# Kernel optimization log

Measured on AMD Instinct MI355X. Metric: run time of the kernel, lower is better.

Reference implementation:

```python
import jax, jax.numpy as jnp
import numpy as np

B, S, D, H, L, E, FF = 16, 1024, 384, 8, 3, 8, 768
DH = D // H
TOP_K = 2


def _ln(x, s, b):
    m = x.mean(-1, keepdims=True)
    v = x.var(-1, keepdims=True)
    return (x - m) * jax.lax.rsqrt(v + 1e-5) * s + b


def setup_inputs() -> dict:
    key = jax.random.key(0)
    ks = jax.random.split(key, 12)
    def n(k, shp, scale=0.02):
        return jax.random.normal(k, shp, jnp.float32) * scale
    return dict(
        x=jax.random.normal(ks[0], (B, S, 1), jnp.float32),
        proj_w=n(ks[1], (1, D)), proj_b=jnp.zeros((D,), jnp.float32),
        qkv_w=n(ks[2], (L, D, 3 * D)), qkv_b=jnp.zeros((L, 3 * D), jnp.float32),
        out_w=n(ks[3], (L, D, D)), out_b=jnp.zeros((L, D), jnp.float32),
        n1_s=jnp.ones((L, D), jnp.float32), n1_b=jnp.zeros((L, D), jnp.float32),
        n2_s=jnp.ones((L, D), jnp.float32), n2_b=jnp.zeros((L, D), jnp.float32),
        gate_w=n(ks[4], (L, D, E)),
        e_w1=n(ks[5], (L, E, D, FF)), e_b1=jnp.zeros((L, E, FF), jnp.float32),
        e_w2=n(ks[6], (L, E, FF, D)), e_b2=jnp.zeros((L, E, D), jnp.float32),
        att_w=n(ks[7], (D,)), att_b=jnp.zeros((), jnp.float32),
        head_w=n(ks[8], (D, 1)), head_b=jnp.zeros((1,), jnp.float32),
    )


def reference(x, proj_w, proj_b, qkv_w, qkv_b, out_w, out_b,
              n1_s, n1_b, n2_s, n2_b, gate_w, e_w1, e_b1, e_w2, e_b2,
              att_w, att_b, head_w, head_b):
    # feature projection: [B,S,1] -> [B,S,D]
    h = x @ proj_w + proj_b
    total_moe = jnp.zeros((), h.dtype)
    scale = np.float32(1.0 / np.sqrt(DH))
    for l in range(L):
        # --- pre-norm multi-head self-attention ---
        xn = _ln(h, n1_s[l], n1_b[l])
        qkv = xn @ qkv_w[l] + qkv_b[l]
        q, k, v = jnp.split(qkv, 3, axis=-1)
        q = q.reshape(B, S, H, DH)
        k = k.reshape(B, S, H, DH)
        v = v.reshape(B, S, H, DH)
        attn = jax.nn.softmax(jnp.einsum('bqhd,bkhd->bhqk', q, k) * scale, axis=-1)
        ao = jnp.einsum('bhqk,bkhd->bqhd', attn, v).reshape(B, S, D)
        h = h + (ao @ out_w[l] + out_b[l])
        # --- pre-norm top-2 gated MoE FFN ---
        xn2 = _ln(h, n2_s[l], n2_b[l])
        probs = jax.nn.softmax(xn2 @ gate_w[l], axis=-1)            # [B,S,E]
        topv, topi = jax.lax.top_k(probs, TOP_K)
        gates = topv / topv.sum(-1, keepdims=True)                  # renormalized top-2
        full = (jax.nn.one_hot(topi, E, dtype=h.dtype) * gates[..., None]).sum(-2)  # [B,S,E]
        moe_out = jnp.zeros_like(h)
        for e in range(E):  # fixed small expert loop
            ye = jax.nn.relu(xn2 @ e_w1[l, e] + e_b1[l, e]) @ e_w2[l, e] + e_b2[l, e]
            moe_out = moe_out + full[..., e:e + 1] * ye
        h = h + moe_out
        # switch-style load-balancing aux loss
        importance = probs.reshape(-1, E).mean(0)
        load = (full > 0).astype(h.dtype).reshape(-1, E).mean(0)
        total_moe = total_moe + E * jnp.sum(importance * load)
    w = jax.nn.softmax(h @ att_w + att_b, axis=1)                   # [B,S]
    pooled = jnp.einsum('bs,bsd->bd', w, h)
    rul = pooled @ head_w + head_b                                  # [B,1]
    return rul, total_moe
```

## Files before the change

### kernel.cpp

```cpp
#include <hip/hip_runtime.h>
#include <hip/hip_bf16.h>
#include <math.h>

#define TOKENS 16384
#define DMODEL 384
#define SEQ 1024
#define NHEAD 8
#define DHEAD 48
#define NEXP 8
#define FFDIM 768
#define NL 3

typedef __bf16 bf16x8 __attribute__((ext_vector_type(8)));
typedef __bf16 bf16x4 __attribute__((ext_vector_type(4)));
typedef float f32x4 __attribute__((ext_vector_type(4)));

__global__ void finalize_kernel(const int* __restrict__ counts_all,
                                const float* __restrict__ sp_all, float* __restrict__ out) {
  float tm = 0.f;
  for (int l = 0; l < NL; l++) {
    float t = 0.f;
    for (int e = 0; e < NEXP; e++)
      t += sp_all[l * NEXP + e] * (float)counts_all[l * NEXP + e];
    tm += (float)NEXP * t / ((float)TOKENS * (float)TOKENS);
  }
  out[16] = tm;
}

__global__ __launch_bounds__(256) void proj_kernel(const float* __restrict__ x,
    const float* __restrict__ pw, const float* __restrict__ pb, float* __restrict__ h) {
  int i = blockIdx.x * 256 + threadIdx.x;
  int t = i / DMODEL;
  int d = i - t * DMODEL;
  h[i] = x[t] * pw[d] + pb[d];
}

__global__ __launch_bounds__(256) void convw_kernel(const float* __restrict__ src,
    __bf16* __restrict__ dst, int K, int N) {
  __shared__ float t[32][33];
  size_t boff = (size_t)blockIdx.z * K * N;
  src += boff; dst += boff;
  int k0 = blockIdx.y * 32, n0 = blockIdx.x * 32;
  int tx = threadIdx.x & 31, ty = threadIdx.x >> 5;
#pragma unroll
  for (int i = 0; i < 32; i += 8) t[ty + i][tx] = src[(size_t)(k0 + ty + i) * N + n0 + tx];
  __syncthreads();
#pragma unroll
  for (int i = 0; i < 32; i += 8)
    dst[(size_t)(n0 + ty + i) * K + k0 + tx] = (__bf16)t[tx][ty + i];
}

__global__ __launch_bounds__(384) void ln_kernel(const float* __restrict__ src,
    __bf16* __restrict__ dst, const float* __restrict__ gs, const float* __restrict__ gb,
    int* __restrict__ zc, float* __restrict__ zs) {
  int row = blockIdx.x, tid = threadIdx.x;
  if (zc && row == 0 && tid < NEXP) { zc[tid] = 0; zs[tid] = 0.f; }
  float v = src[(size_t)row * DMODEL + tid];
  float sum = v, sq = v * v;
#pragma unroll
  for (int off = 32; off; off >>= 1) { sum += __shfl_xor(sum, off); sq += __shfl_xor(sq, off); }
  __shared__ float rs[6], rq[6];
  __shared__ float smean, sinv;
  int wid = tid >> 6;
  if ((tid & 63) == 0) { rs[wid] = sum; rq[wid] = sq; }
  __syncthreads();
  if (tid == 0) {
    float S = 0.f, Q = 0.f;
    for (int w = 0; w < 6; w++) { S += rs[w]; Q += rq[w]; }
    float mean = S / (float)DMODEL;
    float var = Q / (float)DMODEL - mean * mean;
    smean = mean; sinv = rsqrtf(var + 1e-5f);
  }
  __syncthreads();
  dst[(size_t)row * DMODEL + tid] = (__bf16)((v - smean) * sinv * gs[tid] + gb[tid]);
}

__global__ __launch_bounds__(384) void lncomb_kernel(float* __restrict__ h,
    const __bf16* __restrict__ ab, __bf16* __restrict__ dst,
    const float* __restrict__ gs, const float* __restrict__ gb) {
  int row = blockIdx.x, tid = threadIdx.x;
  size_t idx = (size_t)row * DMODEL + tid;
  float v = h[idx] + (float)ab[idx] + (float)ab[(size_t)TOKENS * DMODEL + idx];
  h[idx] = v;
  float sum = v, sq = v * v;
#pragma unroll
  for (int off = 32; off; off >>= 1) { sum += __shfl_xor(sum, off); sq += __shfl_xor(sq, off); }
  __shared__ float rs[6], rq[6];
  __shared__ float smean, sinv;
  int wid = tid >> 6;
  if ((tid & 63) == 0) { rs[wid] = sum; rq[wid] = sq; }
  __syncthreads();
  if (tid == 0) {
    float S = 0.f, Q = 0.f;
    for (int w = 0; w < 6; w++) { S += rs[w]; Q += rq[w]; }
    float mean = S / (float)DMODEL;
    float var = Q / (float)DMODEL - mean * mean;
    smean = mean; sinv = rsqrtf(var + 1e-5f);
  }
  __syncthreads();
  dst[idx] = (__bf16)((v - smean) * sinv * gs[tid] + gb[tid]);
}

template<int MODE>
__global__ __launch_bounds__(256) void mgemm_kernel(
    const __bf16* __restrict__ Abf, const __bf16* __restrict__ Wt,
    const float* __restrict__ bias, float* __restrict__ Cf, __bf16* __restrict__ Cb,
    __bf16* __restrict__ pQ, __bf16* __restrict__ pK, __bf16* __restrict__ pV,
    const int* __restrict__ counts,
    const int* __restrict__ tok_list, const float* __restrict__ gate_list,
    int N, int K) {
  int e = 0, cnt = 0, base = 0;
  const int* tl = nullptr;
  int m0 = blockIdx.y * 128;
  int n0 = blockIdx.x * 128;
  if constexpr (MODE == 2 || MODE == 3) {
    e = blockIdx.z;
    cnt = counts[e];
    if (m0 >= cnt) return;
    for (int i = 0; i < NEXP; i++) {
      int ci = counts[i];
      if (i < e) base += (ci + 63) & ~63;
    }
    tl = tok_list + e * TOKENS;
    Wt += (size_t)e * N * K;
    bias += (size_t)e * N;
  }
  __shared__ __align__(16) __bf16 smem[128][130];
  auto Bs = reinterpret_cast<__bf16(*)[72]>(&smem[0][0]);
  int tid = threadIdx.x;
  int w = tid >> 6, lane = tid & 63, c = lane & 15, g = lane >> 4;
  int arow[4], acol[4];
#pragma unroll
  for (int i = 0; i < 4; i++) {
    int chunk = tid + 256 * i;
    arow[i] = chunk >> 3;
    acol[i] = (chunk & 7) * 8;
  }
  int r1 = w * 32 + c, r2 = r1 + 16;
  long tokf0, tokf1;
  {
    int mr1 = m0 + r1, mr2 = m0 + r2;
    if constexpr (MODE == 2) {
      tokf0 = (mr1 < cnt) ? (long)(tl[mr1] & 0xFFFF) : -1;
      tokf1 = (mr2 < cnt) ? (long)(tl[mr2] & 0xFFFF) : -1;
    } else if constexpr (MODE == 3) {
      tokf0 = (mr1 < cnt) ? (long)(base + mr1) : -1;
      tokf1 = (mr2 < cnt) ? (long)(base + mr2) : -1;
    } else {
      tokf0 = mr1; tokf1 = mr2;
    }
  }
  f32x4 acc[2][8];
#pragma unroll
  for (int m = 0; m < 2; m++)
#pragma unroll
    for (int n = 0; n < 8; n++) { acc[m][n][0] = 0.f; acc[m][n][1] = 0.f; acc[m][n][2] = 0.f; acc[m][n][3] = 0.f; }

  bf16x8 rb[4];
  bf16x8 af0a = {}, af0b = {}, af1a = {}, af1b = {};
  int nk = K >> 6;
#pragma unroll
  for (int i = 0; i < 4; i++)
    rb[i] = *(const bf16x8*)&Wt[(size_t)(n0 + arow[i]) * K + acol[i]];
  if (tokf0 >= 0) {
    af0a = *(const bf16x8*)&Abf[(size_t)tokf0 * K + g * 8];
    af0b = *(const bf16x8*)&Abf[(size_t)tokf0 * K + 32 + g * 8];
  }
  if (tokf1 >= 0) {
    af1a = *(const bf16x8*)&Abf[(size_t)tokf1 * K + g * 8];
    af1b = *(const bf16x8*)&Abf[(size_t)tokf1 * K + 32 + g * 8];
  }
  for (int kt = 0; kt < nk; kt++) {
#pragma unroll
    for (int i = 0; i < 4; i++)
      *(bf16x8*)&Bs[arow[i]][acol[i]] = rb[i];
    __syncthreads();
    int k0 = (kt + 1) << 6;
    if (kt + 1 < nk) {
#pragma unroll
      for (int i = 0; i < 4; i++)
        rb[i] = *(const bf16x8*)&Wt[(size_t)(n0 + arow[i]) * K + k0 + acol[i]];
    }
#pragma unroll
    for (int n = 0; n < 8; n++) {
      bf16x8 b0 = *(const bf16x8*)&Bs[n * 16 + c][g * 8];
      acc[0][n] = __builtin_amdgcn_mfma_f32_16x16x32_bf16(af0a, b0, acc[0][n], 0, 0, 0);
      acc[1][n] = __builtin_amdgcn_mfma_f32_16x16x32_bf16(af1a, b0, acc[1][n], 0, 0, 0);
    }
#pragma unroll
    for (int n = 0; n < 8; n++) {
      bf16x8 b1 = *(const bf16x8*)&Bs[n * 16 + c][32 + g * 8];
      acc[0][n] = __builtin_amdgcn_mfma_f32_16x16x32_bf16(af0b, b1, acc[0][n], 0, 0, 0);
      acc[1][n] = __builtin_amdgcn_mfma_f32_16x16x32_bf16(af1b, b1, acc[1][n], 0, 0, 0);
    }
    if (kt + 1 < nk) {
      if (tokf0 >= 0) {
        af0a = *(const bf16x8*)&Abf[(size_t)tokf0 * K + k0 + g * 8];
        af0b = *(const bf16x8*)&Abf[(size_t)tokf0 * K + k0 + 32 + g * 8];
      }
      if (tokf1 >= 0) {
        af1a = *(const bf16x8*)&Abf[(size_t)tokf1 * K + k0 + g * 8];
        af1b = *(const bf16x8*)&Abf[(size_t)tokf1 * K + k0 + 32 + g * 8];
      }
    }
    __syncthreads();
  }
  if constexpr (MODE == 1) {
#pragma unroll
    for (int m = 0; m < 2; m++) {
      int row = w * 32 + m * 16 + 4 * g;
#pragma unroll
      for (int n = 0; n < 8; n++) {
        int col = n0 + n * 16 + c;
        float bv = bias[col];
#pragma unroll
        for (int r = 0; r < 4; r++)
          Cf[(size_t)(m0 + row + r) * N + col] += acc[m][n][r] + bv;
      }
    }
  } else if constexpr (MODE == 0) {
    __bf16* Ct = &smem[0][0];
    const int CSTR = 130;
    int which = n0 / 384;
    int rem0 = n0 - which * 384;
#pragma unroll
    for (int m = 0; m < 2; m++) {
      int row = w * 32 + m * 16 + 4 * g;
#pragma unroll
      for (int n = 0; n < 8; n++) {
        int col = n * 16 + c;
        float bv = bias[n0 + col];
#pragma unroll
        for (int r = 0; r < 4; r++) {
          float v = acc[m][n][r] + bv;
          if (which == 0) v *= 0.20823510262f;
          Ct[(row + r) * CSTR + col] = (__bf16)v;
        }
      }
    }
    __syncthreads();
    int b0 = m0 >> 10, sbase = m0 & 1023;
    if (which < 2) {
      __bf16* dstbuf = (which == 0) ? pQ : pK;
#pragma unroll
      for (int it = 0; it < 4; it++) {
        int ch = it * 256 + tid;
        int row = ch >> 3, seg = ch & 7;
        int rem = rem0 + seg * 16;
        int hd = rem / 48, d = rem - hd * 48;
        size_t bh = (size_t)(b0 * 8 + hd);
        __bf16* dst = &dstbuf[(bh * 1024 + sbase + row) * 48 + d];
        const __bf16* srcl = &Ct[row * CSTR + seg * 16];
        *(bf16x8*)&dst[0] = *(const bf16x8*)&srcl[0];
        *(bf16x8*)&dst[8] = *(const bf16x8*)&srcl[8];
      }
    } else {
      int col = tid >> 1, half = tid & 1;
      int rem = rem0 + col;
      int hd = rem / 48, d = rem - hd * 48;
      size_t bh = (size_t)(b0 * 8 + hd);
      __bf16* dst = &pV[(bh * 48 + d) * 1024 + sbase + half * 64];
      const __bf16* srcc = &Ct[(half * 64) * CSTR + col];
#pragma unroll
      for (int i8 = 0; i8 < 8; i8++) {
        bf16x8 vv;
#pragma unroll
        for (int j = 0; j < 8; j++) vv[j] = srcc[(i8 * 8 + j) * CSTR];
        *(bf16x8*)&dst[i8 * 8] = vv;
      }
    }
  } else {
    __bf16* Ct = &smem[0][0];
    const int CSTR = 130;
    float rowg[2][4];
    if constexpr (MODE == 3) {
#pragma unroll
      for (int m = 0; m < 2; m++)
#pragma unroll
        for (int r = 0; r < 4; r++) {
          int row = m0 + w * 32 + m * 16 + 4 * g + r;
          rowg[m][r] = (row < cnt) ? gate_list[e * TOKENS + row] : 0.f;
        }
    }
#pragma unroll
    for (int m = 0; m < 2; m++) {
      int row = w * 32 + m * 16 + 4 * g;
#pragma unroll
      for (int n = 0; n < 8; n++) {
        int col = n * 16 + c;
        float bv = bias[n0 + col];
#pragma unroll
        for (int r = 0; r < 4; r++) {
          float v = acc[m][n][r] + bv;
          if constexpr (MODE == 2) v = fmaxf(v, 0.f);
          else v *= rowg[m][r];
          Ct[(row + r) * CSTR + col] = (__bf16)v;
        }
      }
    }
    __syncthreads();
    int row = tid >> 1, half = tid & 1;
    int mr = m0 + row;
    if (mr < cnt) {
      const __bf16* srcl = &Ct[row * CSTR + half * 64];
      __bf16* dst;
      if constexpr (MODE == 2) {
        dst = &Cb[(size_t)(base + mr) * N + n0 + half * 64];
      } else {
        int entry = tl[mr];
        int t = entry & 0xFFFF, a = entry >> 16;
        dst = &Cb[((size_t)a * TOKENS + t) * DMODEL + n0 + half * 64];
      }
#pragma unroll
      for (int i = 0; i < 8; i++) *(bf16x8*)&dst[i * 8] = *(const bf16x8*)&srcl[i * 8];
    }
  }
}

__global__ __launch_bounds__(256) void combine_kernel(float* __restrict__ h,
    const __bf16* __restrict__ ab) {
  size_t i = ((size_t)blockIdx.x * 256 + threadIdx.x) * 8;
  bf16x8 a0 = *(const bf16x8*)&ab[i];
  bf16x8 a1 = *(const bf16x8*)&ab[(size_t)TOKENS * DMODEL + i];
  float* hp = h + i;
#pragma unroll
  for (int j = 0; j < 8; j++) hp[j] += (float)a0[j] + (float)a1[j];
}

__global__ __launch_bounds__(256, 4) void attn_kernel(const __bf16* __restrict__ Qh,
    const __bf16* __restrict__ Kh, const __bf16* __restrict__ VTh,
    __bf16* __restrict__ ao) {
  __shared__ __align__(16) __bf16 Ks[64][72];
  __shared__ __align__(16) __bf16 Vt[48][72];
  __shared__ __align__(16) __bf16 Ps[4][2][16][72];
  int bh = blockIdx.x;
  int q0 = blockIdx.y * 128;
  int tid = threadIdx.x;
  int w = tid >> 6, lane = tid & 63, c = lane & 15, g = lane >> 4;

  for (int i = tid; i < 192; i += 256) {
    int row = i / 3, seg = i - row * 3;
    bf16x8 z = {};
    *(bf16x8*)&Ks[row][48 + seg * 8] = z;
  }

  const __bf16* qrowA = Qh + ((size_t)bh * 1024 + q0 + w * 16 + c) * 48;
  const __bf16* qrowB = qrowA + 64 * 48;
  bf16x8 qb0a = *(const bf16x8*)&qrowA[g * 8];
  bf16x8 qb0b = *(const bf16x8*)&qrowB[g * 8];
  bf16x8 qb1a = {}, qb1b = {};
  if (g < 2) {
    qb1a = *(const bf16x8*)&qrowA[32 + g * 8];
    qb1b = *(const bf16x8*)&qrowB[32 + g * 8];
  }

  const __bf16* kb = Kh + (size_t)bh * 1024 * 48;
  const __bf16* vb = VTh + (size_t)bh * 48 * 1024;

  int r0 = tid / 6, p0 = tid - r0 * 6;
  __bf16* dst0 = &Ks[r0][p0 * 8];
  int off0 = r0 * 48 + p0 * 8;
  int e1 = tid + 256;
  __bf16* dst1; int off1; bool v1;
  if (e1 < 384) { int r = e1 / 6, p = e1 - r * 6; dst1 = &Ks[r][p * 8]; off1 = r * 48 + p * 8; v1 = false; }
  else          { int i = e1 - 384; int d = i >> 3, p = i & 7; dst1 = &Vt[d][p * 8]; off1 = d * 1024 + p * 8; v1 = true; }
  int i2 = tid + 512 - 384;
  int d2 = i2 >> 3, p2 = i2 & 7;
  __bf16* dst2 = &Vt[d2][p2 * 8];
  int off2 = d2 * 1024 + p2 * 8;

  f32x4 accA[3] = {}, accB[3] = {};
  f32x4 laccA = {}, laccB = {};
  bf16x8 ones;
#pragma unroll
  for (int j = 0; j < 8; j++) ones[j] = (__bf16)1.0f;

  for (int kt = 0; kt < 16; kt++) {
    __syncthreads();
    const __bf16* kbt = kb + (size_t)kt * 3072;
    const __bf16* vbt = vb + kt * 64;
    *(bf16x8*)dst0 = *(const bf16x8*)(kbt + off0);
    *(bf16x8*)dst1 = *(const bf16x8*)((v1 ? vbt : kbt) + off1);
    *(bf16x8*)dst2 = *(const bf16x8*)(vbt + off2);
    __syncthreads();

#pragma unroll
    for (int f = 0; f < 4; f++) {
      bf16x8 ka0 = *(const bf16x8*)&Ks[f * 16 + c][g * 8];
      bf16x8 ka1 = *(const bf16x8*)&Ks[f * 16 + c][32 + g * 8];
      f32x4 za = {}, zb = {};
      za = __builtin_amdgcn_mfma_f32_16x16x32_bf16(ka0, qb0a, za, 0, 0, 0);
      f32x4 sa = __builtin_amdgcn_mfma_f32_16x16x32_bf16(ka1, qb1a, za, 0, 0, 0);
      zb = __builtin_amdgcn_mfma_f32_16x16x32_bf16(ka0, qb0b, zb, 0, 0, 0);
      f32x4 sb = __builtin_amdgcn_mfma_f32_16x16x32_bf16(ka1, qb1b, zb, 0, 0, 0);
      bf16x4 pka = { (__bf16)__builtin_amdgcn_exp2f(sa[0]), (__bf16)__builtin_amdgcn_exp2f(sa[1]),
                     (__bf16)__builtin_amdgcn_exp2f(sa[2]), (__bf16)__builtin_amdgcn_exp2f(sa[3]) };
      bf16x4 pkb = { (__bf16)__builtin_amdgcn_exp2f(sb[0]), (__bf16)__builtin_amdgcn_exp2f(sb[1]),
                     (__bf16)__builtin_amdgcn_exp2f(sb[2]), (__bf16)__builtin_amdgcn_exp2f(sb[3]) };
      *(bf16x4*)&Ps[w][0][c][f * 16 + 4 * g] = pka;
      *(bf16x4*)&Ps[w][1][c][f * 16 + 4 * g] = pkb;
    }
    bf16x8 pa0a = *(const bf16x8*)&Ps[w][0][c][g * 8];
    bf16x8 pa1a = *(const bf16x8*)&Ps[w][0][c][32 + g * 8];
    bf16x8 pa0b = *(const bf16x8*)&Ps[w][1][c][g * 8];
    bf16x8 pa1b = *(const bf16x8*)&Ps[w][1][c][32 + g * 8];
#pragma unroll
    for (int t = 0; t < 3; t++) {
      bf16x8 vb0 = *(const bf16x8*)&Vt[t * 16 + c][g * 8];
      bf16x8 vb1 = *(const bf16x8*)&Vt[t * 16 + c][32 + g * 8];
      accA[t] = __builtin_amdgcn_mfma_f32_16x16x32_bf16(pa0a, vb0, accA[t], 0, 0, 0);
      accA[t] = __builtin_amdgcn_mfma_f32_16x16x32_bf16(pa1a, vb1, accA[t], 0, 0, 0);
      accB[t] = __builtin_amdgcn_mfma_f32_16x16x32_bf16(pa0b, vb0, accB[t], 0, 0, 0);
      accB[t] = __builtin_amdgcn_mfma_f32_16x16x32_bf16(pa1b, vb1, accB[t], 0, 0, 0);
    }
    laccA = __builtin_amdgcn_mfma_f32_16x16x32_bf16(pa0a, ones, laccA, 0, 0, 0);
    laccA = __builtin_amdgcn_mfma_f32_16x16x32_bf16(pa1a, ones, laccA, 0, 0, 0);
    laccB = __builtin_amdgcn_mfma_f32_16x16x32_bf16(pa0b, ones, laccB, 0, 0, 0);
    laccB = __builtin_amdgcn_mfma_f32_16x16x32_bf16(pa1b, ones, laccB, 0, 0, 0);
  }
  float linvA[4], linvB[4];
#pragma unroll
  for (int r = 0; r < 4; r++) { linvA[r] = 1.f / laccA[r]; linvB[r] = 1.f / laccB[r]; }
  int b = bh >> 3, hh = bh & 7;
#pragma unroll
  for (int t = 0; t < 3; t++)
#pragma unroll
    for (int r = 0; r < 4; r++) {
      size_t rowA = (size_t)(b * SEQ + q0 + w * 16 + 4 * g + r);
      ao[rowA * DMODEL + hh * 48 + t * 16 + c] = (__bf16)(accA[t][r] * linvA[r]);
      ao[(rowA + 64) * DMODEL + hh * 48 + t * 16 + c] = (__bf16)(accB[t][r] * linvB[r]);
    }
}

__global__ __launch_bounds__(256) void gate_kernel(const __bf16* __restrict__ xnb,
    const float* __restrict__ gw, int* __restrict__ counts, float* __restrict__ sum_probs,
    int* __restrict__ tok_list, float* __restrict__ gate_list) {
  __shared__ float Gs[NEXP][DMODEL];
  __shared__ float simp[NEXP];
  __shared__ int hist[NEXP], basep[NEXP];
  __shared__ unsigned char tokE[32][2];
  __shared__ float tokG[32][2];
  __shared__ short rankS[32][2];
  int tid = threadIdx.x;
  for (int i = tid; i < DMODEL * NEXP; i += 256) {
    int d = i >> 3, e2 = i & 7;
    Gs[e2][d] = gw[i];
  }
  if (tid < NEXP) { simp[tid] = 0.f; hist[tid] = 0; }
  __syncthreads();
  int w = tid >> 6, lane = tid & 63;
  int tbase = blockIdx.x * 32 + w * 8;
  float impacc[NEXP] = {};
  for (int tt = 0; tt < 8; tt++) {
    int t = tbase + tt;
    float p[NEXP] = {};
#pragma unroll
    for (int j = 0; j < 6; j++) {
      int d = lane + 64 * j;
      float xv = (float)xnb[(size_t)t * DMODEL + d];
#pragma unroll
      for (int e2 = 0; e2 < NEXP; e2++) p[e2] += xv * Gs[e2][d];
    }
#pragma unroll
    for (int off = 32; off; off >>= 1)
#pragma unroll
      for (int e2 = 0; e2 < NEXP; e2++) p[e2] += __shfl_xor(p[e2], off);
    float mx = p[0];
#pragma unroll
    for (int e2 = 1; e2 < NEXP; e2++) mx = fmaxf(mx, p[e2]);
    float s = 0.f;
#pragma unroll
    for (int e2 = 0; e2 < NEXP; e2++) { p[e2] = __expf(p[e2] - mx); s += p[e2]; }
    float inv = 1.f / s;
#pragma unroll
    for (int e2 = 0; e2 < NEXP; e2++) { p[e2] *= inv; impacc[e2] += p[e2]; }
    int i0 = 0; float v0 = p[0];
#pragma unroll
    for (int e2 = 1; e2 < NEXP; e2++) if (p[e2] > v0) { v0 = p[e2]; i0 = e2; }
    int i1 = -1; float v1 = -INFINITY;
#pragma unroll
    for (int e2 = 0; e2 < NEXP; e2++) if (e2 != i0 && p[e2] > v1) { v1 = p[e2]; i1 = e2; }
    if (lane == 0) {
      float gsum = v0 + v1;
      int r0 = atomicAdd(&hist[i0], 1);
      int r1 = atomicAdd(&hist[i1], 1);
      int sl = w * 8 + tt;
      tokE[sl][0] = (unsigned char)i0; tokE[sl][1] = (unsigned char)i1;
      tokG[sl][0] = v0 / gsum;         tokG[sl][1] = v1 / gsum;
      rankS[sl][0] = (short)r0;        rankS[sl][1] = (short)r1;
    }
  }
  if (lane == 0)
#pragma unroll
    for (int e2 = 0; e2 < NEXP; e2++) atomicAdd(&simp[e2], impacc[e2]);
  __syncthreads();
  if (tid < NEXP) {
    basep[tid] = atomicAdd(&counts[tid], hist[tid]);
    atomicAdd(&sum_probs[tid], simp[tid]);
  }
  __syncthreads();
  int t0 = blockIdx.x * 32;
  if (tid < 64) {
    int sl = tid >> 1, a = tid & 1;
    int e2 = tokE[sl][a];
    int pos = basep[e2] + rankS[sl][a];
    tok_list[e2 * TOKENS + pos] = (t0 + sl) | (a << 16);
    gate_list[e2 * TOKENS + pos] = tokG[sl][a];
  }
}

__global__ __launch_bounds__(256) void head1_kernel(const float* __restrict__ h,
    const float* __restrict__ att_w, const float* __restrict__ att_b,
    float* __restrict__ logits) {
  int tid = threadIdx.x;
  int w = tid >> 6, lane = tid & 63;
  float4 aw0 = *(const float4*)&att_w[lane * 4];
  float2 aw1 = *(const float2*)&att_w[256 + lane * 2];
  float ab = att_b[0];
  for (int i = w; i < 32; i += 4) {
    int t = blockIdx.x * 32 + i;
    const float* hr = h + (size_t)t * DMODEL;
    float4 v4 = *(const float4*)&hr[lane * 4];
    float2 v2 = *(const float2*)&hr[256 + lane * 2];
    float dot = v4.x * aw0.x + v4.y * aw0.y + v4.z * aw0.z + v4.w * aw0.w
              + v2.x * aw1.x + v2.y * aw1.y;
#pragma unroll
    for (int off = 32; off; off >>= 1) dot += __shfl_xor(dot, off);
    if (lane == 0) logits[t] = dot + ab;
  }
}

__global__ __launch_bounds__(256) void head2_kernel(float* __restrict__ logits) {
  int b = blockIdx.x, tid = threadIdx.x;
  int w = tid >> 6, lane = tid & 63;
  float* lb = logits + b * SEQ;
  __shared__ float red[4];
  float lv[4];
  float mx = -INFINITY;
#pragma unroll
  for (int i = 0; i < 4; i++) { lv[i] = lb[tid + 256 * i]; mx = fmaxf(mx, lv[i]); }
#pragma unroll
  for (int off = 32; off; off >>= 1) mx = fmaxf(mx, __shfl_xor(mx, off));
  if (lane == 0) red[w] = mx;
  __syncthreads();
  mx = fmaxf(fmaxf(red[0], red[1]), fmaxf(red[2], red[3]));
  __syncthreads();
  float s = 0.f;
#pragma unroll
  for (int i = 0; i < 4; i++) { lv[i] = __expf(lv[i] - mx); s += lv[i]; }
#pragma unroll
  for (int off = 32; off; off >>= 1) s += __shfl_xor(s, off);
  if (lane == 0) red[w] = s;
  __syncthreads();
  float inv = 1.f / (red[0] + red[1] + red[2] + red[3]);
#pragma unroll
  for (int i = 0; i < 4; i++) lb[tid + 256 * i] = lv[i] * inv;
}

__global__ __launch_bounds__(256) void head3a_kernel(const float* __restrict__ h,
    const float* __restrict__ wnorm, float* __restrict__ partial) {
  int b = blockIdx.x, dc = blockIdx.y, sc = blockIdx.z;
  int tid = threadIdx.x;
  int d = tid & 63, sg = tid >> 6;
  const float* hb = h + (size_t)b * SEQ * DMODEL + dc * 64 + d;
  const float* wb = wnorm + b * SEQ + sc * 64;
  float acc = 0.f;
  int s0 = sc * 64 + sg * 16;
#pragma unroll
  for (int i = 0; i < 16; i++)
    acc += wb[sg * 16 + i] * hb[(size_t)(s0 + i) * DMODEL];
  __shared__ float red[256];
  red[tid] = acc;
  __syncthreads();
  if (sg == 0)
    partial[(((size_t)b * 6 + dc) * 16 + sc) * 64 + d] =
        red[d] + red[64 + d] + red[128 + d] + red[192 + d];
}

__global__ void head3b_kernel(const float* __restrict__ partial,
    const float* __restrict__ head_w, float* __restrict__ part) {
  int b = blockIdx.x, dc = blockIdx.y;
  int d = threadIdx.x;
  const float* pp = partial + (((size_t)b * 6 + dc) * 16) * 64 + d;
  float pooled = 0.f;
#pragma unroll
  for (int sc = 0; sc < 16; sc++) pooled += pp[sc * 64];
  float pd = pooled * head_w[dc * 64 + d];
#pragma unroll
  for (int off = 32; off; off >>= 1) pd += __shfl_xor(pd, off);
  if (d == 0) part[b * 6 + dc] = pd;
}

__global__ void head4_kernel(const float* __restrict__ part,
                             const float* __restrict__ head_b, float* __restrict__ out) {
  int b = threadIdx.x;
  if (b < 16) {
    float s = head_b[0];
#pragma unroll
    for (int dc = 0; dc < 6; dc++) s += part[b * 6 + dc];
    out[b] = s;
  }
}

extern "C" void kernel_launch(void* const* d_in, const int* in_sizes, int n_in,
                              void* d_out, int out_size, void* d_ws, size_t ws_size,
                              hipStream_t stream) {
  (void)in_sizes; (void)n_in; (void)out_size; (void)ws_size;
  const float* x      = (const float*)d_in[0];
  const float* proj_w = (const float*)d_in[1];
  const float* proj_b = (const float*)d_in[2];
  const float* qkv_w  = (const float*)d_in[3];
  const float* qkv_b  = (const float*)d_in[4];
  const float* out_w  = (const float*)d_in[5];
  const float* out_b  = (const float*)d_in[6];
  const float* n1_s   = (const float*)d_in[7];
  const float* n1_b   = (const float*)d_in[8];
  const float* n2_s   = (const float*)d_in[9];
  const float* n2_b   = (const float*)d_in[10];
  const float* gate_w = (const float*)d_in[11];
  const float* e_w1   = (const float*)d_in[12];
  const float* e_b1   = (const float*)d_in[13];
  const float* e_w2   = (const float*)d_in[14];
  const float* e_b2   = (const float*)d_in[15];
  const float* att_w  = (const float*)d_in[16];
  const float* att_b  = (const float*)d_in[17];
  const float* head_w = (const float*)d_in[18];
  const float* head_b = (const float*)d_in[19];
  float* out = (float*)d_out;

  char* wsb = (char*)d_ws;
  float*  h    = (float*)(wsb);
  __bf16* xnb  = (__bf16*)(wsb + 25165824);
  __bf16* aob  = (__bf16*)(wsb + 37748736);
  __bf16* ab   = (__bf16*)(wsb + 25165824);
  __bf16* uni  = (__bf16*)(wsb + 50331648);
  __bf16* Qh   = uni;
  __bf16* Khd  = (__bf16*)(wsb + 62914560);
  __bf16* VTh  = (__bf16*)(wsb + 75497472);
  __bf16* qkvWt = (__bf16*)(wsb + 101449728);
  __bf16* outWt = (__bf16*)(wsb + 104103936);
  __bf16* e1Wt  = (__bf16*)(wsb + 104988672);
  __bf16* e2Wt  = (__bf16*)(wsb + 119144448);
  char* sm = wsb + 133300224;
  int*   counts_all = (int*)(sm);
  float* sp_all     = (float*)(sm + 128);
  int*   tok_list  = (int*)(sm + 256);
  float* gate_list = (float*)(sm + 256 + 524288);
  float* logits    = (float*)(sm + 1048832);
  float* part      = (float*)(sm + 1048832 + 65536);
  float* partial   = (float*)(sm + 1048832 + 131072);

  convw_kernel<<<dim3(36, 12, 3), 256, 0, stream>>>(qkv_w, qkvWt, 384, 1152);
  convw_kernel<<<dim3(12, 12, 3), 256, 0, stream>>>(out_w, outWt, 384, 384);
  convw_kernel<<<dim3(24, 12, 24), 256, 0, stream>>>(e_w1, e1Wt, 384, 768);
  convw_kernel<<<dim3(12, 24, 24), 256, 0, stream>>>(e_w2, e2Wt, 768, 384);

  proj_kernel<<<TOKENS * DMODEL / 256, 256, 0, stream>>>(x, proj_w, proj_b, h);
  ln_kernel<<<TOKENS, 384, 0, stream>>>(h, xnb, n1_s, n1_b, nullptr, nullptr);

  for (int l = 0; l < NL; l++) {
    int*   counts = counts_all + l * NEXP;
    float* sp     = sp_all + l * NEXP;
    mgemm_kernel<0><<<dim3(9, 128), 256, 0, stream>>>(
        xnb, qkvWt + (size_t)l * 1152 * 384, qkv_b + l * 1152, nullptr, nullptr,
        Qh, Khd, VTh, nullptr, nullptr, nullptr, 1152, 384);
    attn_kernel<<<dim3(128, 8), 256, 0, stream>>>(Qh, Khd, VTh, aob);
    mgemm_kernel<1><<<dim3(3, 128), 256, 0, stream>>>(
        aob, outWt + (size_t)l * 384 * 384, out_b + l * 384, h, nullptr,
        nullptr, nullptr, nullptr, nullptr, nullptr, nullptr, 384, 384);
    ln_kernel<<<TOKENS, 384, 0, stream>>>(h, xnb, n2_s + l * DMODEL, n2_b + l * DMODEL,
                                          counts, sp);
    gate_kernel<<<512, 256, 0, stream>>>(xnb, gate_w + (size_t)l * DMODEL * NEXP,
                                         counts, sp, tok_list, gate_list);
    mgemm_kernel<2><<<dim3(6, 128, 8), 256, 0, stream>>>(
        xnb, e1Wt + (size_t)l * 8 * 768 * 384, e_b1 + l * 8 * FFDIM, nullptr, uni,
        nullptr, nullptr, nullptr, counts, tok_list, nullptr, 768, 384);
    mgemm_kernel<3><<<dim3(3, 128, 8), 256, 0, stream>>>(
        uni, e2Wt + (size_t)l * 8 * 384 * 768, e_b2 + l * 8 * DMODEL, nullptr, ab,
        nullptr, nullptr, nullptr, counts, tok_list, gate_list, 384, 768);
    if (l + 1 < NL) {
      lncomb_kernel<<<TOKENS, 384, 0, stream>>>(h, ab, xnb,
          n1_s + (l + 1) * DMODEL, n1_b + (l + 1) * DMODEL);
    } else {
      combine_kernel<<<TOKENS * DMODEL / (256 * 8), 256, 0, stream>>>(h, ab);
    }
  }

  head1_kernel<<<512, 256, 0, stream>>>(h, att_w, att_b, logits);
  head2_kernel<<<16, 256, 0, stream>>>(logits);
  head3a_kernel<<<dim3(16, 6, 16), 256, 0, stream>>>(h, logits, partial);
  head3b_kernel<<<dim3(16, 6), 64, 0, stream>>>(partial, head_w, part);
  head4_kernel<<<1, 64, 0, stream>>>(part, head_b, out);
  finalize_kernel<<<1, 1, 0, stream>>>(counts_all, sp_all, out);
}
```

Baseline: 873.6 us.

## Load expert GEMM weights directly from global memory, skipping LDS staging

For the MoE expert GEMM modes (2 and 3), the weight tile is no longer staged through shared memory with barriers. Each wave instead reads its B fragments straight from global memory (served by L1/L2) and issues MFMAs without any __syncthreads. Mode 1 also gets a smaller shared array, and modes 0/1 drop the token-validity branches on A loads. The aim is to remove barrier stalls and raise occupancy, at the cost of redundant global weight reads across the four waves and no software prefetch.

```diff
diff --git a/kernel.cpp b/kernel.cpp
--- a/kernel.cpp
+++ b/kernel.cpp
@@ -125,7 +125,8 @@
     Wt += (size_t)e * N * K;
     bias += (size_t)e * N;
   }
-  __shared__ __align__(16) __bf16 smem[128][130];
+  constexpr int SW = (MODE == 1) ? 72 : 130;
+  __shared__ __align__(16) __bf16 smem[128][SW];
   auto Bs = reinterpret_cast<__bf16(*)[72]>(&smem[0][0]);
   int tid = threadIdx.x;
   int w = tid >> 6, lane = tid & 63, c = lane & 15, g = lane >> 4;
@@ -156,54 +157,79 @@
 #pragma unroll
     for (int n = 0; n < 8; n++) { acc[m][n][0] = 0.f; acc[m][n][1] = 0.f; acc[m][n][2] = 0.f; acc[m][n][3] = 0.f; }
 
-  bf16x8 rb[4];
-  bf16x8 af0a = {}, af0b = {}, af1a = {}, af1b = {};
   int nk = K >> 6;
-#pragma unroll
-  for (int i = 0; i < 4; i++)
-    rb[i] = *(const bf16x8*)&Wt[(size_t)(n0 + arow[i]) * K + acol[i]];
-  if (tokf0 >= 0) {
+  if constexpr (MODE <= 1) {
+    bf16x8 rb[4];
+    bf16x8 af0a = {}, af0b = {}, af1a = {}, af1b = {};
+#pragma unroll
+    for (int i = 0; i < 4; i++)
+      rb[i] = *(const bf16x8*)&Wt[(size_t)(n0 + arow[i]) * K + acol[i]];
     af0a = *(const bf16x8*)&Abf[(size_t)tokf0 * K + g * 8];
     af0b = *(const bf16x8*)&Abf[(size_t)tokf0 * K + 32 + g * 8];
-  }
-  if (tokf1 >= 0) {
     af1a = *(const bf16x8*)&Abf[(size_t)tokf1 * K + g * 8];
     af1b = *(const bf16x8*)&Abf[(size_t)tokf1 * K + 32 + g * 8];
-  }
-  for (int kt = 0; kt < nk; kt++) {
-#pragma unroll
-    for (int i = 0; i < 4; i++)
-      *(bf16x8*)&Bs[arow[i]][acol[i]] = rb[i];
-    __syncthreads();
-    int k0 = (kt + 1) << 6;
-    if (kt + 1 < nk) {
+    for (int kt = 0; kt < nk; kt++) {
 #pragma unroll
       for (int i = 0; i < 4; i++)
-        rb[i] = *(const bf16x8*)&Wt[(size_t)(n0 + arow[i]) * K + k0 + acol[i]];
-    }
-#pragma unroll
-    for (int n = 0; n < 8; n++) {
-      bf16x8 b0 = *(const bf16x8*)&Bs[n * 16 + c][g * 8];
-      acc[0][n] = __builtin_amdgcn_mfma_f32_16x16x32_bf16(af0a, b0, acc[0][n], 0, 0, 0);
-      acc[1][n] = __builtin_amdgcn_mfma_f32_16x16x32_bf16(af1a, b0, acc[1][n], 0, 0, 0);
-    }
-#pragma unroll
-    for (int n = 0; n < 8; n++) {
-      bf16x8 b1 = *(const bf16x8*)&Bs[n * 16 + c][32 + g * 8];
-      acc[0][n] = __builtin_amdgcn_mfma_f32_16x16x32_bf16(af0b, b1, acc[0][n], 0, 0, 0);
-      acc[1][n] = __builtin_amdgcn_mfma_f32_16x16x32_bf16(af1b, b1, acc[1][n], 0, 0, 0);
-    }
-    if (kt + 1 < nk) {
-      if (tokf0 >= 0) {
+        *(bf16x8*)&Bs[arow[i]][acol[i]] = rb[i];
+      __syncthreads();
+      int k0 = (kt + 1) << 6;
+      if (kt + 1 < nk) {
+#pragma unroll
+        for (int i = 0; i < 4; i++)
+          rb[i] = *(const bf16x8*)&Wt[(size_t)(n0 + arow[i]) * K + k0 + acol[i]];
+      }
+#pragma unroll
+      for (int n = 0; n < 8; n++) {
+        bf16x8 b0 = *(const bf16x8*)&Bs[n * 16 + c][g * 8];
+        acc[0][n] = __builtin_amdgcn_mfma_f32_16x16x32_bf16(af0a, b0, acc[0][n], 0, 0, 0);
+        acc[1][n] = __builtin_amdgcn_mfma_f32_16x16x32_bf16(af1a, b0, acc[1][n], 0, 0, 0);
+      }
+#pragma unroll
+      for (int n = 0; n < 8; n++) {
+        bf16x8 b1 = *(const bf16x8*)&Bs[n * 16 + c][32 + g * 8];
+        acc[0][n] = __builtin_amdgcn_mfma_f32_16x16x32_bf16(af0b, b1, acc[0][n], 0, 0, 0);
+        acc[1][n] = __builtin_amdgcn_mfma_f32_16x16x32_bf16(af1b, b1, acc[1][n], 0, 0, 0);
+      }
+      if (kt + 1 < nk) {
         af0a = *(const bf16x8*)&Abf[(size_t)tokf0 * K + k0 + g * 8];
         af0b = *(const bf16x8*)&Abf[(size_t)tokf0 * K + k0 + 32 + g * 8];
-      }
-      if (tokf1 >= 0) {
         af1a = *(const bf16x8*)&Abf[(size_t)tokf1 * K + k0 + g * 8];
         af1b = *(const bf16x8*)&Abf[(size_t)tokf1 * K + k0 + 32 + g * 8];
       }
-    }
-    __syncthreads();
+      __syncthreads();
+    }
+  } else {
+    for (int kt = 0; kt < nk; kt++) {
+      int kb = kt << 6;
+      bf16x8 a0a = {}, a0b = {}, a1a = {}, a1b = {};
+      if (tokf0 >= 0) {
+        a0a = *(const bf16x8*)&Abf[(size_t)tokf0 * K + kb + g * 8];
+        a0b = *(const bf16x8*)&Abf[(size_t)tokf0 * K + kb + 32 + g * 8];
+      }
+      if (tokf1 >= 0) {
+        a1a = *(const bf16x8*)&Abf[(size_t)tokf1 * K + kb + g * 8];
+        a1b = *(const bf16x8*)&Abf[(size_t)tokf1 * K + kb + 32 + g * 8];
+      }
+#pragma unroll
+      for (int half = 0; half < 2; half++) {
+        bf16x8 bf0[4], bf1[4];
+#pragma unroll
+        for (int j = 0; j < 4; j++) {
+          const __bf16* wp = &Wt[(size_t)(n0 + (half * 4 + j) * 16 + c) * K + kb];
+          bf0[j] = *(const bf16x8*)&wp[g * 8];
+          bf1[j] = *(const bf16x8*)&wp[32 + g * 8];
+        }
+#pragma unroll
+        for (int j = 0; j < 4; j++) {
+          int n = half * 4 + j;
+          acc[0][n] = __builtin_amdgcn_mfma_f32_16x16x32_bf16(a0a, bf0[j], acc[0][n], 0, 0, 0);
+          acc[1][n] = __builtin_amdgcn_mfma_f32_16x16x32_bf16(a1a, bf0[j], acc[1][n], 0, 0, 0);
+          acc[0][n] = __builtin_amdgcn_mfma_f32_16x16x32_bf16(a0b, bf1[j], acc[0][n], 0, 0, 0);
+          acc[1][n] = __builtin_amdgcn_mfma_f32_16x16x32_bf16(a1b, bf1[j], acc[1][n], 0, 0, 0);
+        }
+      }
+    }
   }
   if constexpr (MODE == 1) {
 #pragma unroll
```

After: 1.312 ms. +50.2%, slower.
